# Performance work log

Measured on AMD Instinct MI355X. Metric: run time of the kernel, lower is better.

Reference implementation:

```python
import jax, jax.numpy as jnp
import numpy as np

WS = 7      # window size
NH = 8      # num heads

def setup_inputs() -> dict:
    key = jax.random.key(0)
    k1, k2, k3 = jax.random.split(key, 3)
    B, H, W, C = 32, 56, 56, 256
    x = jax.random.normal(k1, (B, H, W, C), dtype=jnp.float32)
    w_qkv = jax.random.normal(k2, (3 * C, C), dtype=jnp.float32) * 0.02
    w_proj = jax.random.normal(k3, (C, C), dtype=jnp.float32) * 0.02
    b_proj = jnp.zeros((C,), dtype=jnp.float32)
    return {"x": x, "w_qkv": w_qkv, "w_proj": w_proj, "b_proj": b_proj}

def reference(x, w_qkv, w_proj, b_proj):
    B, H, W, C = x.shape
    hd = C // NH
    scale = hd ** -0.5
    # window partition: (B,H,W,C) -> (nW, ws^2, C)
    xw = x.reshape(B, H // WS, WS, W // WS, WS, C)
    xw = xw.transpose(0, 1, 3, 2, 4, 5).reshape(-1, WS * WS, C)
    # fused qkv projection (no bias)
    qkv = (xw @ w_qkv.T).reshape(-1, WS * WS, 3, NH, hd)
    q, k, v = qkv[:, :, 0], qkv[:, :, 1], qkv[:, :, 2]  # (nW, ws^2, nh, hd)
    # NOTE: faithful to source quirk — contraction over head_dim per token,
    # producing an (nh x nh) head-mixing attention matrix per token.
    attn = jnp.einsum('nshd,nsed->nshe', q, k) * scale   # (nW, ws^2, nh, nh)
    attn = jax.nn.softmax(attn, axis=-1)
    out = jnp.einsum('nshe,nsed->nshd', attn, v)         # (nW, ws^2, nh, hd)
    # source does transpose(1,2).reshape(-1, ws^2, C) — replicate exactly
    out = out.swapaxes(1, 2).reshape(-1, WS * WS, C)
    out = out @ w_proj.T + b_proj
    # window un-partition
    out = out.reshape(B, H // WS, W // WS, WS, WS, C)
    out = out.transpose(0, 1, 3, 2, 4, 5).reshape(B, H, W, C)
    return out
```

## Files before the change

### kernel.cpp

```cpp
#include <hip/hip_runtime.h>
#include <hip/hip_bf16.h>

typedef __bf16 bf16_t;
typedef bf16_t bf16x8 __attribute__((ext_vector_type(8)));
typedef float floatx4 __attribute__((ext_vector_type(4)));

#define MFMA16(a, b, c) __builtin_amdgcn_mfma_f32_16x16x32_bf16((a), (b), (c), 0, 0, 0)

__global__ __launch_bounds__(256) void wconv_kernel(
    const float* __restrict__ w_qkv, const float* __restrict__ w_proj,
    bf16_t* __restrict__ wb)
{
  int i = blockIdx.x * 256 + threadIdx.x;
  const float* src;
  bf16_t* dst;
  if (i < 24576) {
    int chunk = i >> 6, l = i & 63;
    int p = chunk >> 5, rem = chunk & 31, k = rem >> 2, j = rem & 3;
    int col = p * 64 + j * 16 + (l & 15);
    int kk = k * 32 + (l >> 4) * 8;
    src = w_qkv + col * 256 + kk;
    dst = wb + (i << 3);
  } else {
    int ip = i - 24576;
    int chunk = ip >> 6, l = ip & 63;
    int p = chunk >> 4, rem = chunk & 15, k = rem >> 1, j = rem & 1;
    int col = p * 32 + j * 16 + (l & 15);
    int kk = k * 32 + (l >> 4) * 8;
    src = w_proj + col * 256 + kk;
    dst = wb + 196608 + (ip << 3);
  }
  float4 f0 = ((const float4*)src)[0];
  float4 f1 = ((const float4*)src)[1];
  bf16_t t8[8] = {(bf16_t)f0.x, (bf16_t)f0.y, (bf16_t)f0.z, (bf16_t)f0.w,
                  (bf16_t)f1.x, (bf16_t)f1.y, (bf16_t)f1.z, (bf16_t)f1.w};
  *(uint4*)dst = *(const uint4*)t8;
}

__device__ __forceinline__ void cvt8_store(bf16_t* dst, float4 f0, float4 f1) {
  bf16_t t8[8] = {(bf16_t)f0.x, (bf16_t)f0.y, (bf16_t)f0.z, (bf16_t)f0.w,
                  (bf16_t)f1.x, (bf16_t)f1.y, (bf16_t)f1.z, (bf16_t)f1.w};
  *(uint4*)dst = *(const uint4*)t8;
}

#define XS_S 272
#define QK_S 520

__global__ __launch_bounds__(512, 4) void attn_kernel(
    const float* __restrict__ x,
    const bf16_t* __restrict__ wb,
    float* __restrict__ outf,
    bf16_t* __restrict__ preb)
{
  __shared__ __align__(16) bf16_t Xs[32][XS_S];
  __shared__ __align__(16) bf16_t QK[32][QK_S];

  const int tid = threadIdx.x;
  const int wave = tid >> 6, lane = tid & 63, quad = lane >> 4, l16 = lane & 15;
  const long base = (long)blockIdx.x * 32;
  const float scale = 0.17677669529663687f;

  auto loadB = [&](bf16x8* dst, int pan, int k) {
    const bf16_t* c = wb + ((long)(pan * 32 + k * 4) << 9) + lane * 8;
#pragma unroll
    for (int j = 0; j < 4; ++j) dst[j] = *(const bf16x8*)(c + (j << 9));
  };

  const float* xb = x + base * 256;
#pragma unroll
  for (int it = 0; it < 2; ++it) {
    int idx = tid + it * 512;
    int s = idx >> 5, g = (idx & 31) * 8;
    const float* p = xb + s * 256 + g;
    float4 f0 = ((const float4*)p)[0];
    float4 f1 = ((const float4*)p)[1];
    cvt8_store(&Xs[s][g], f0, f1);
  }
  __syncthreads();

  {
    floatx4 acc[2][4] = {};
    bf16x8 Ba[4], Bb[4];
    loadB(Ba, wave, 0);
#pragma unroll
    for (int k = 0; k < 8; ++k) {
      const bf16x8* cur = (k & 1) ? Bb : Ba;
      if (k < 7) loadB((k & 1) ? Ba : Bb, wave, k + 1);
      bf16x8 A0 = *(const bf16x8*)(&Xs[l16][k * 32 + quad * 8]);
      bf16x8 A1 = *(const bf16x8*)(&Xs[16 + l16][k * 32 + quad * 8]);
#pragma unroll
      for (int j = 0; j < 4; ++j) {
        acc[0][j] = MFMA16(A0, cur[j], acc[0][j]);
        acc[1][j] = MFMA16(A1, cur[j], acc[1][j]);
      }
    }
#pragma unroll
    for (int i = 0; i < 2; ++i)
#pragma unroll
      for (int j = 0; j < 4; ++j)
#pragma unroll
        for (int r = 0; r < 4; ++r)
          QK[i * 16 + quad * 4 + r][wave * 64 + j * 16 + l16] = (bf16_t)acc[i][j][r];
  }
  __syncthreads();

  float p_[8];
  floatx4 vacc[2][4];
  if (wave < 4) {
    const int t = tid >> 3, h = tid & 7;
    bf16x8 qv[4];
#pragma unroll
    for (int u = 0; u < 4; ++u) qv[u] = *(const bf16x8*)(&QK[t][h * 32 + u * 8]);
    float qf[32];
#pragma unroll
    for (int u = 0; u < 4; ++u)
#pragma unroll
      for (int d = 0; d < 8; ++d) qf[u * 8 + d] = (float)qv[u][d];
    float sc[8];
#pragma unroll
    for (int eh = 0; eh < 2; ++eh) {
      bf16x8 kv[4][4];
#pragma unroll
      for (int e2 = 0; e2 < 4; ++e2)
#pragma unroll
        for (int u = 0; u < 4; ++u)
          kv[e2][u] = *(const bf16x8*)(&QK[t][256 + (eh * 4 + e2) * 32 + u * 8]);
#pragma unroll
      for (int e2 = 0; e2 < 4; ++e2) {
        float a = 0.f;
#pragma unroll
        for (int u = 0; u < 4; ++u)
#pragma unroll
          for (int d = 0; d < 8; ++d) a += qf[u * 8 + d] * (float)kv[e2][u][d];
        sc[eh * 4 + e2] = a;
      }
    }
    float mx = -INFINITY;
#pragma unroll
    for (int e = 0; e < 8; ++e) { sc[e] *= scale; mx = fmaxf(mx, sc[e]); }
    float sum = 0.f;
#pragma unroll
    for (int e = 0; e < 8; ++e) { p_[e] = __expf(sc[e] - mx); sum += p_[e]; }
    float rs = 1.0f / sum;
#pragma unroll
    for (int e = 0; e < 8; ++e) p_[e] *= rs;
  } else {
    const int pan = 8 + (wave - 4);
#pragma unroll
    for (int i = 0; i < 2; ++i)
#pragma unroll
      for (int j = 0; j < 4; ++j) vacc[i][j] = (floatx4){0.f, 0.f, 0.f, 0.f};
    bf16x8 Ba[4], Bb[4];
    loadB(Ba, pan, 0);
#pragma unroll
    for (int k = 0; k < 8; ++k) {
      const bf16x8* cur = (k & 1) ? Bb : Ba;
      if (k < 7) loadB((k & 1) ? Ba : Bb, pan, k + 1);
      bf16x8 A0 = *(const bf16x8*)(&Xs[l16][k * 32 + quad * 8]);
      bf16x8 A1 = *(const bf16x8*)(&Xs[16 + l16][k * 32 + quad * 8]);
#pragma unroll
      for (int j = 0; j < 4; ++j) {
        vacc[0][j] = MFMA16(A0, cur[j], vacc[0][j]);
        vacc[1][j] = MFMA16(A1, cur[j], vacc[1][j]);
      }
    }
  }
  __syncthreads();

  if (wave >= 4) {
    const int u = wave - 4;
#pragma unroll
    for (int i = 0; i < 2; ++i)
#pragma unroll
      for (int j = 0; j < 4; ++j)
#pragma unroll
        for (int r = 0; r < 4; ++r)
          QK[i * 16 + quad * 4 + r][u * 64 + j * 16 + l16] = (bf16_t)vacc[i][j][r];
  }
  __syncthreads();

  if (wave < 4) {
    const int t = tid >> 3, h = tid & 7;
    float pre[32];
#pragma unroll
    for (int i = 0; i < 32; ++i) pre[i] = 0.f;
#pragma unroll
    for (int eh = 0; eh < 2; ++eh) {
      bf16x8 vv[4][4];
#pragma unroll
      for (int e2 = 0; e2 < 4; ++e2)
#pragma unroll
        for (int u = 0; u < 4; ++u)
          vv[e2][u] = *(const bf16x8*)(&QK[t][(eh * 4 + e2) * 32 + u * 8]);
#pragma unroll
      for (int e2 = 0; e2 < 4; ++e2) {
        float pe = p_[eh * 4 + e2];
#pragma unroll
        for (int u = 0; u < 4; ++u)
#pragma unroll
          for (int d = 0; d < 8; ++d) pre[u * 8 + d] += pe * (float)vv[e2][u][d];
      }
    }
    if (preb) {
      bf16_t* op = preb + (base + t) * 256 + h * 32;
#pragma unroll
      for (int u = 0; u < 4; ++u) {
        bf16_t t8[8];
#pragma unroll
        for (int d = 0; d < 8; ++d) t8[d] = (bf16_t)pre[u * 8 + d];
        *(uint4*)(op + u * 8) = *(const uint4*)t8;
      }
    } else {
      float* op = outf + (base + t) * 256 + h * 32;
#pragma unroll
      for (int u = 0; u < 8; ++u) {
        float4 f = {pre[u * 4], pre[u * 4 + 1], pre[u * 4 + 2], pre[u * 4 + 3]};
        ((float4*)op)[u] = f;
      }
    }
  }
}

#define SC_S 264

__global__ __launch_bounds__(512, 4) void proj_kernel(
    const bf16_t* __restrict__ wb,
    const float* __restrict__ b_proj,
    float* out,
    const bf16_t* __restrict__ preb)
{
  __shared__ __align__(16) bf16_t Sc[49][SC_S];
  __shared__ int trow[49];

  const int n = blockIdx.x;
  const int b = n >> 6, wh = (n >> 3) & 7, ww = n & 7;
  const int tid = threadIdx.x;
  const int wave = tid >> 6, lane = tid & 63, quad = lane >> 4, l16 = lane & 15;

  auto loadB2 = [&](bf16x8 (*dst)[2], int k0) {
#pragma unroll
    for (int kk = 0; kk < 4; ++kk)
#pragma unroll
      for (int j = 0; j < 2; ++j)
        dst[kk][j] = *(const bf16x8*)(wb + 196608 +
            ((long)(wave * 16 + (k0 + kk) * 2 + j) << 9) + lane * 8);
  };
  bf16x8 Bh0[4][2];
  loadB2(Bh0, 0);
  float bv[2];
#pragma unroll
  for (int j = 0; j < 2; ++j) bv[j] = b_proj[wave * 32 + j * 16 + l16];

  if (tid < 49) {
    int i = tid / 7, j = tid % 7;
    trow[tid] = b * 3136 + (wh * 7 + i) * 56 + ww * 7 + j;
  }
  __syncthreads();

  if (preb) {
    for (int idx = tid; idx < 49 * 32; idx += 512) {
      int s = idx >> 5, g8 = idx & 31;
      bf16x8 v = *(const bf16x8*)(preb + (long)trow[s] * 256 + g8 * 8);
      int flat = (g8 >> 2) * 1568 + s * 32 + (g8 & 3) * 8;
      *(bf16x8*)(&Sc[flat >> 8][flat & 255]) = v;
    }
  } else {
    for (int idx = tid; idx < 49 * 32; idx += 512) {
      int s = idx >> 5, g8 = idx & 31;
      const float* p = out + (long)trow[s] * 256 + g8 * 8;
      float4 f0 = ((const float4*)p)[0];
      float4 f1 = ((const float4*)p)[1];
      int flat = (g8 >> 2) * 1568 + s * 32 + (g8 & 3) * 8;
      cvt8_store(&Sc[flat >> 8][flat & 255], f0, f1);
    }
  }
  bf16x8 Bh1[4][2];
  loadB2(Bh1, 4);
  __syncthreads();

  {
    floatx4 acc[4][2] = {};
    bf16x8 Aa[4], Ab[4];
    auto loadA = [&](bf16x8* dst, int k) {
#pragma unroll
      for (int i = 0; i < 4; ++i) {
        int mr = i * 16 + l16; if (mr > 48) mr = 48;
        dst[i] = *(const bf16x8*)(&Sc[mr][k * 32 + quad * 8]);
      }
    };
    loadA(Aa, 0);
#pragma unroll
    for (int k = 0; k < 8; ++k) {
      const bf16x8* curA = (k & 1) ? Ab : Aa;
      if (k < 7) loadA((k & 1) ? Aa : Ab, k + 1);
#pragma unroll
      for (int i = 0; i < 4; ++i)
#pragma unroll
        for (int j = 0; j < 2; ++j)
          acc[i][j] = MFMA16(curA[i], (k < 4) ? Bh0[k][j] : Bh1[k - 4][j], acc[i][j]);
    }
#pragma unroll
    for (int j = 0; j < 2; ++j) {
      int col = wave * 32 + j * 16 + l16;
#pragma unroll
      for (int i = 0; i < 4; ++i)
#pragma unroll
        for (int r = 0; r < 4; ++r) {
          int m = i * 16 + quad * 4 + r;
          if (m < 49) out[(long)trow[m] * 256 + col] = acc[i][j][r] + bv[j];
        }
    }
  }
}

extern "C" void kernel_launch(void* const* d_in, const int* in_sizes, int n_in,
                              void* d_out, int out_size, void* d_ws, size_t ws_size,
                              hipStream_t stream) {
  (void)in_sizes; (void)n_in; (void)out_size;
  const float* x      = (const float*)d_in[0];
  const float* w_qkv  = (const float*)d_in[1];
  const float* w_proj = (const float*)d_in[2];
  const float* b_proj = (const float*)d_in[3];
  float* out = (float*)d_out;
  bf16_t* wb = (bf16_t*)d_ws;

  bf16_t* preb = nullptr;
  if (ws_size >= (size_t)524288 + 51380224) preb = wb + 262144;

  wconv_kernel<<<dim3(128), 256, 0, stream>>>(w_qkv, w_proj, wb);
  attn_kernel<<<dim3(3136), 512, 0, stream>>>(x, wb, out, preb);
  proj_kernel<<<dim3(2048), 512, 0, stream>>>(wb, b_proj, out, preb);
}
```

Measured before the change: 279.9 us.

## Compute QKV in one MFMA pass, split head-mix across lanes, gather proj A directly

The attention kernel now has all 8 waves compute 96 of the 768 QKV columns each in a single GEMM pass, with V written into the reused Xs buffer. This replaces the earlier split where half the waves idled during the V GEMM. The head-mixing softmax is split across two lanes per (token, head) using a shuffle reduction, and the probabilities are stored in shared memory as fp16. The P·V step is spread across all 512 threads instead of only 256. The projection kernel drops the shared-memory staging and gathers its A operands straight from the bf16 intermediate with the transposed indexing, at the cost of scattered global loads and per-element division arithmetic.

```diff
diff --git a/kernel.cpp b/kernel.cpp
--- a/kernel.cpp
+++ b/kernel.cpp
@@ -16,8 +16,8 @@
   bf16_t* dst;
   if (i < 24576) {
     int chunk = i >> 6, l = i & 63;
-    int p = chunk >> 5, rem = chunk & 31, k = rem >> 2, j = rem & 3;
-    int col = p * 64 + j * 16 + (l & 15);
+    int c = chunk >> 3, k = chunk & 7;
+    int col = c * 16 + (l & 15);
     int kk = k * 32 + (l >> 4) * 8;
     src = w_qkv + col * 256 + kk;
     dst = wb + (i << 3);
@@ -43,7 +43,7 @@
   *(uint4*)dst = *(const uint4*)t8;
 }
 
-#define XS_S 272
+#define XS_S 264
 #define QK_S 520
 
 __global__ __launch_bounds__(512, 4) void attn_kernel(
@@ -54,17 +54,12 @@
 {
   __shared__ __align__(16) bf16_t Xs[32][XS_S];
   __shared__ __align__(16) bf16_t QK[32][QK_S];
+  __shared__ __align__(16) _Float16 Pl[32][8][8];
 
   const int tid = threadIdx.x;
   const int wave = tid >> 6, lane = tid & 63, quad = lane >> 4, l16 = lane & 15;
   const long base = (long)blockIdx.x * 32;
   const float scale = 0.17677669529663687f;
-
-  auto loadB = [&](bf16x8* dst, int pan, int k) {
-    const bf16_t* c = wb + ((long)(pan * 32 + k * 4) << 9) + lane * 8;
-#pragma unroll
-    for (int j = 0; j < 4; ++j) dst[j] = *(const bf16x8*)(c + (j << 9));
-  };
 
   const float* xb = x + base * 256;
 #pragma unroll
@@ -78,239 +73,274 @@
   }
   __syncthreads();
 
+  floatx4 acc[2][6];
+#pragma unroll
+  for (int i = 0; i < 2; ++i)
+#pragma unroll
+    for (int j = 0; j < 6; ++j) acc[i][j] = (floatx4){0.f, 0.f, 0.f, 0.f};
   {
-    floatx4 acc[2][4] = {};
-    bf16x8 Ba[4], Bb[4];
-    loadB(Ba, wave, 0);
+    auto loadB6 = [&](bf16x8 (&dst)[6], int k) {
+      const bf16_t* cb = wb + ((long)(wave * 48 + k) << 9) + lane * 8;
+#pragma unroll
+      for (int j = 0; j < 6; ++j) dst[j] = *(const bf16x8*)(cb + (j << 12));
+    };
+    bf16x8 Ba[6], Bb[6];
+    loadB6(Ba, 0);
 #pragma unroll
     for (int k = 0; k < 8; ++k) {
       const bf16x8* cur = (k & 1) ? Bb : Ba;
-      if (k < 7) loadB((k & 1) ? Ba : Bb, wave, k + 1);
+      if (k < 7) loadB6((k & 1) ? Ba : Bb, k + 1);
       bf16x8 A0 = *(const bf16x8*)(&Xs[l16][k * 32 + quad * 8]);
       bf16x8 A1 = *(const bf16x8*)(&Xs[16 + l16][k * 32 + quad * 8]);
 #pragma unroll
-      for (int j = 0; j < 4; ++j) {
+      for (int j = 0; j < 6; ++j) {
         acc[0][j] = MFMA16(A0, cur[j], acc[0][j]);
         acc[1][j] = MFMA16(A1, cur[j], acc[1][j]);
       }
     }
+  }
+  __syncthreads();
+
+#pragma unroll
+  for (int j = 0; j < 6; ++j) {
+    int g = wave * 96 + j * 16 + l16;
 #pragma unroll
     for (int i = 0; i < 2; ++i)
 #pragma unroll
-      for (int j = 0; j < 4; ++j)
-#pragma unroll
-        for (int r = 0; r < 4; ++r)
-          QK[i * 16 + quad * 4 + r][wave * 64 + j * 16 + l16] = (bf16_t)acc[i][j][r];
-  }
-  __syncthreads();
-
-  float p_[8];
-  floatx4 vacc[2][4];
-  if (wave < 4) {
-    const int t = tid >> 3, h = tid & 7;
-    bf16x8 qv[4];
-#pragma unroll
-    for (int u = 0; u < 4; ++u) qv[u] = *(const bf16x8*)(&QK[t][h * 32 + u * 8]);
-    float qf[32];
-#pragma unroll
-    for (int u = 0; u < 4; ++u)
-#pragma unroll
-      for (int d = 0; d < 8; ++d) qf[u * 8 + d] = (float)qv[u][d];
+      for (int r = 0; r < 4; ++r) {
+        int row = i * 16 + quad * 4 + r;
+        if (g < 512) QK[row][g] = (bf16_t)acc[i][j][r];
+        else         Xs[row][g - 512] = (bf16_t)acc[i][j][r];
+      }
+  }
+  __syncthreads();
+
+  {
+    const int t = tid >> 4, h = (tid >> 1) & 7, sg = tid & 1;
+    const bf16_t* qrow = &QK[t][h * 32 + sg * 16];
+    float qf[16];
+    {
+      bf16x8 q0 = *(const bf16x8*)(qrow);
+      bf16x8 q1 = *(const bf16x8*)(qrow + 8);
+#pragma unroll
+      for (int d = 0; d < 8; ++d) { qf[d] = (float)q0[d]; qf[8 + d] = (float)q1[d]; }
+    }
     float sc[8];
 #pragma unroll
-    for (int eh = 0; eh < 2; ++eh) {
-      bf16x8 kv[4][4];
-#pragma unroll
-      for (int e2 = 0; e2 < 4; ++e2)
-#pragma unroll
-        for (int u = 0; u < 4; ++u)
-          kv[e2][u] = *(const bf16x8*)(&QK[t][256 + (eh * 4 + e2) * 32 + u * 8]);
-#pragma unroll
-      for (int e2 = 0; e2 < 4; ++e2) {
-        float a = 0.f;
-#pragma unroll
-        for (int u = 0; u < 4; ++u)
-#pragma unroll
-          for (int d = 0; d < 8; ++d) a += qf[u * 8 + d] * (float)kv[e2][u][d];
-        sc[eh * 4 + e2] = a;
-      }
-    }
+    for (int e = 0; e < 8; ++e) {
+      const bf16_t* krow = &QK[t][256 + e * 32 + sg * 16];
+      bf16x8 k0 = *(const bf16x8*)(krow);
+      bf16x8 k1 = *(const bf16x8*)(krow + 8);
+      float a = 0.f;
+#pragma unroll
+      for (int d = 0; d < 8; ++d) a += qf[d] * (float)k0[d] + qf[8 + d] * (float)k1[d];
+      sc[e] = a;
+    }
+#pragma unroll
+    for (int e = 0; e < 8; ++e) sc[e] += __shfl_xor(sc[e], 1);
     float mx = -INFINITY;
 #pragma unroll
     for (int e = 0; e < 8; ++e) { sc[e] *= scale; mx = fmaxf(mx, sc[e]); }
-    float sum = 0.f;
-#pragma unroll
-    for (int e = 0; e < 8; ++e) { p_[e] = __expf(sc[e] - mx); sum += p_[e]; }
+    float sum = 0.f, pv[8];
+#pragma unroll
+    for (int e = 0; e < 8; ++e) { pv[e] = __expf(sc[e] - mx); sum += pv[e]; }
     float rs = 1.0f / sum;
-#pragma unroll
-    for (int e = 0; e < 8; ++e) p_[e] *= rs;
-  } else {
-    const int pan = 8 + (wave - 4);
-#pragma unroll
-    for (int i = 0; i < 2; ++i)
-#pragma unroll
-      for (int j = 0; j < 4; ++j) vacc[i][j] = (floatx4){0.f, 0.f, 0.f, 0.f};
-    bf16x8 Ba[4], Bb[4];
-    loadB(Ba, pan, 0);
-#pragma unroll
-    for (int k = 0; k < 8; ++k) {
-      const bf16x8* cur = (k & 1) ? Bb : Ba;
-      if (k < 7) loadB((k & 1) ? Ba : Bb, pan, k + 1);
-      bf16x8 A0 = *(const bf16x8*)(&Xs[l16][k * 32 + quad * 8]);
-      bf16x8 A1 = *(const bf16x8*)(&Xs[16 + l16][k * 32 + quad * 8]);
-#pragma unroll
-      for (int j = 0; j < 4; ++j) {
-        vacc[0][j] = MFMA16(A0, cur[j], vacc[0][j]);
-        vacc[1][j] = MFMA16(A1, cur[j], vacc[1][j]);
-      }
-    }
-  }
-  __syncthreads();
-
-  if (wave >= 4) {
-    const int u = wave - 4;
-#pragma unroll
-    for (int i = 0; i < 2; ++i)
-#pragma unroll
-      for (int j = 0; j < 4; ++j)
-#pragma unroll
-        for (int r = 0; r < 4; ++r)
-          QK[i * 16 + quad * 4 + r][u * 64 + j * 16 + l16] = (bf16_t)vacc[i][j][r];
-  }
-  __syncthreads();
-
-  if (wave < 4) {
-    const int t = tid >> 3, h = tid & 7;
-    float pre[32];
-#pragma unroll
-    for (int i = 0; i < 32; ++i) pre[i] = 0.f;
-#pragma unroll
-    for (int eh = 0; eh < 2; ++eh) {
-      bf16x8 vv[4][4];
-#pragma unroll
-      for (int e2 = 0; e2 < 4; ++e2)
-#pragma unroll
-        for (int u = 0; u < 4; ++u)
-          vv[e2][u] = *(const bf16x8*)(&QK[t][(eh * 4 + e2) * 32 + u * 8]);
-#pragma unroll
-      for (int e2 = 0; e2 < 4; ++e2) {
-        float pe = p_[eh * 4 + e2];
-#pragma unroll
-        for (int u = 0; u < 4; ++u)
-#pragma unroll
-          for (int d = 0; d < 8; ++d) pre[u * 8 + d] += pe * (float)vv[e2][u][d];
+    if (sg == 0) {
+      _Float16 ph[8];
+#pragma unroll
+      for (int e = 0; e < 8; ++e) ph[e] = (_Float16)(pv[e] * rs);
+      *(uint4*)(&Pl[t][h][0]) = *(const uint4*)ph;
+    }
+  }
+  __syncthreads();
+
+  {
+    const int t = tid >> 4, j = tid & 15, j8 = j & 7, h0 = j >> 3;
+    float pf[4][8];
+#pragma unroll
+    for (int m = 0; m < 4; ++m) {
+      _Float16 ph[8];
+      *(uint4*)ph = *(const uint4*)(&Pl[t][h0 + 2 * m][0]);
+#pragma unroll
+      for (int e = 0; e < 8; ++e) pf[m][e] = (float)ph[e];
+    }
+    float pr[4][4];
+#pragma unroll
+    for (int m = 0; m < 4; ++m)
+#pragma unroll
+      for (int d = 0; d < 4; ++d) pr[m][d] = 0.f;
+#pragma unroll
+    for (int e = 0; e < 8; ++e) {
+      bf16_t v4[4];
+      *(uint2*)v4 = *(const uint2*)(&Xs[t][e * 32 + j8 * 4]);
+      float vf[4];
+#pragma unroll
+      for (int d = 0; d < 4; ++d) vf[d] = (float)v4[d];
+#pragma unroll
+      for (int m = 0; m < 4; ++m) {
+        float pe = pf[m][e];
+#pragma unroll
+        for (int d = 0; d < 4; ++d) pr[m][d] += pe * vf[d];
       }
     }
     if (preb) {
-      bf16_t* op = preb + (base + t) * 256 + h * 32;
-#pragma unroll
-      for (int u = 0; u < 4; ++u) {
-        bf16_t t8[8];
-#pragma unroll
-        for (int d = 0; d < 8; ++d) t8[d] = (bf16_t)pre[u * 8 + d];
-        *(uint4*)(op + u * 8) = *(const uint4*)t8;
+      bf16_t* op = preb + (base + t) * 256 + j * 4;
+#pragma unroll
+      for (int m = 0; m < 4; ++m) {
+        bf16_t o4[4] = {(bf16_t)pr[m][0], (bf16_t)pr[m][1],
+                        (bf16_t)pr[m][2], (bf16_t)pr[m][3]};
+        *(uint2*)(op + m * 64) = *(const uint2*)o4;
       }
     } else {
-      float* op = outf + (base + t) * 256 + h * 32;
-#pragma unroll
-      for (int u = 0; u < 8; ++u) {
-        float4 f = {pre[u * 4], pre[u * 4 + 1], pre[u * 4 + 2], pre[u * 4 + 3]};
-        ((float4*)op)[u] = f;
-      }
-    }
-  }
-}
-
-#define SC_S 264
+      float* op = outf + (base + t) * 256 + j * 4;
+#pragma unroll
+      for (int m = 0; m < 4; ++m) {
+        float4 f = {pr[m][0], pr[m][1], pr[m][2], pr[m][3]};
+        *(float4*)(op + m * 64) = f;
+      }
+    }
+  }
+}
 
 __global__ __launch_bounds__(512, 4) void proj_kernel(
     const bf16_t* __restrict__ wb,
     const float* __restrict__ b_proj,
-    float* out,
+    float* __restrict__ out,
     const bf16_t* __restrict__ preb)
+{
+  const int n = blockIdx.x;
+  const int b = n >> 6, wh = (n >> 3) & 7, ww = n & 7;
+  const int rowbase = b * 3136 + wh * 392 + ww * 7;
+  const int tid = threadIdx.x;
+  const int wave = tid >> 6, lane = tid & 63, quad = lane >> 4, l16 = lane & 15;
+
+  auto loadBp = [&](bf16x8 (&dst)[2], int k) {
+#pragma unroll
+    for (int j = 0; j < 2; ++j)
+      dst[j] = *(const bf16x8*)(wb + 196608 +
+          ((long)(wave * 16 + k * 2 + j) << 9) + lane * 8);
+  };
+  auto loadA = [&](bf16x8 (&dst)[4], int k) {
+#pragma unroll
+    for (int i = 0; i < 4; ++i) {
+      int mr = i * 16 + l16; if (mr > 48) mr = 48;
+      int q5 = mr * 8 + k;
+      int h = q5 / 49;
+      int s = q5 - h * 49;
+      int srow = (s / 7) * 56 + (s - (s / 7) * 7);
+      dst[i] = *(const bf16x8*)(preb + (long)(rowbase + srow) * 256 +
+                                h * 32 + quad * 8);
+    }
+  };
+
+  const float bv0 = b_proj[wave * 32 + l16];
+  const float bv1 = b_proj[wave * 32 + 16 + l16];
+
+  floatx4 acc[4][2];
+#pragma unroll
+  for (int i = 0; i < 4; ++i)
+#pragma unroll
+    for (int j = 0; j < 2; ++j) acc[i][j] = (floatx4){0.f, 0.f, 0.f, 0.f};
+
+  bf16x8 Aa[4], Ab[4], Ba[2], Bb[2];
+  loadA(Aa, 0); loadBp(Ba, 0);
+#pragma unroll
+  for (int k = 0; k < 8; ++k) {
+    const bf16x8* cA = (k & 1) ? Ab : Aa;
+    const bf16x8* cB = (k & 1) ? Bb : Ba;
+    if (k < 7) { loadA((k & 1) ? Aa : Ab, k + 1); loadBp((k & 1) ? Ba : Bb, k + 1); }
+#pragma unroll
+    for (int i = 0; i < 4; ++i) {
+      acc[i][0] = MFMA16(cA[i], cB[0], acc[i][0]);
+      acc[i][1] = MFMA16(cA[i], cB[1], acc[i][1]);
+    }
+  }
+#pragma unroll
+  for (int i = 0; i < 4; ++i)
+#pragma unroll
+    for (int r = 0; r < 4; ++r) {
+      int m = i * 16 + quad * 4 + r;
+      if (m < 49) {
+        int srow = (m / 7) * 56 + (m - (m / 7) * 7);
+        float* orow = out + (long)(rowbase + srow) * 256 + wave * 32 + l16;
+        orow[0]  = acc[i][0][r] + bv0;
+        orow[16] = acc[i][1][r] + bv1;
+      }
+    }
+}
+
+#define SC_S 264
+__global__ __launch_bounds__(512, 4) void proj_fallback(
+    const bf16_t* __restrict__ wb,
+    const float* __restrict__ b_proj,
+    float* out)
 {
   __shared__ __align__(16) bf16_t Sc[49][SC_S];
   __shared__ int trow[49];
-
   const int n = blockIdx.x;
   const int b = n >> 6, wh = (n >> 3) & 7, ww = n & 7;
   const int tid = threadIdx.x;
   const int wave = tid >> 6, lane = tid & 63, quad = lane >> 4, l16 = lane & 15;
 
-  auto loadB2 = [&](bf16x8 (*dst)[2], int k0) {
-#pragma unroll
-    for (int kk = 0; kk < 4; ++kk)
-#pragma unroll
-      for (int j = 0; j < 2; ++j)
-        dst[kk][j] = *(const bf16x8*)(wb + 196608 +
-            ((long)(wave * 16 + (k0 + kk) * 2 + j) << 9) + lane * 8);
+  auto loadBp = [&](bf16x8 (&dst)[2], int k) {
+#pragma unroll
+    for (int j = 0; j < 2; ++j)
+      dst[j] = *(const bf16x8*)(wb + 196608 +
+          ((long)(wave * 16 + k * 2 + j) << 9) + lane * 8);
   };
-  bf16x8 Bh0[4][2];
-  loadB2(Bh0, 0);
-  float bv[2];
-#pragma unroll
-  for (int j = 0; j < 2; ++j) bv[j] = b_proj[wave * 32 + j * 16 + l16];
+  const float bv0 = b_proj[wave * 32 + l16];
+  const float bv1 = b_proj[wave * 32 + 16 + l16];
 
   if (tid < 49) {
     int i = tid / 7, j = tid % 7;
     trow[tid] = b * 3136 + (wh * 7 + i) * 56 + ww * 7 + j;
   }
   __syncthreads();
-
-  if (preb) {
-    for (int idx = tid; idx < 49 * 32; idx += 512) {
-      int s = idx >> 5, g8 = idx & 31;
-      bf16x8 v = *(const bf16x8*)(preb + (long)trow[s] * 256 + g8 * 8);
-      int flat = (g8 >> 2) * 1568 + s * 32 + (g8 & 3) * 8;
-      *(bf16x8*)(&Sc[flat >> 8][flat & 255]) = v;
-    }
-  } else {
-    for (int idx = tid; idx < 49 * 32; idx += 512) {
-      int s = idx >> 5, g8 = idx & 31;
-      const float* p = out + (long)trow[s] * 256 + g8 * 8;
-      float4 f0 = ((const float4*)p)[0];
-      float4 f1 = ((const float4*)p)[1];
-      int flat = (g8 >> 2) * 1568 + s * 32 + (g8 & 3) * 8;
-      cvt8_store(&Sc[flat >> 8][flat & 255], f0, f1);
-    }
-  }
-  bf16x8 Bh1[4][2];
-  loadB2(Bh1, 4);
-  __syncthreads();
-
-  {
-    floatx4 acc[4][2] = {};
-    bf16x8 Aa[4], Ab[4];
-    auto loadA = [&](bf16x8* dst, int k) {
-#pragma unroll
-      for (int i = 0; i < 4; ++i) {
-        int mr = i * 16 + l16; if (mr > 48) mr = 48;
-        dst[i] = *(const bf16x8*)(&Sc[mr][k * 32 + quad * 8]);
-      }
-    };
-    loadA(Aa, 0);
-#pragma unroll
-    for (int k = 0; k < 8; ++k) {
-      const bf16x8* curA = (k & 1) ? Ab : Aa;
-      if (k < 7) loadA((k & 1) ? Aa : Ab, k + 1);
-#pragma unroll
-      for (int i = 0; i < 4; ++i)
-#pragma unroll
-        for (int j = 0; j < 2; ++j)
-          acc[i][j] = MFMA16(curA[i], (k < 4) ? Bh0[k][j] : Bh1[k - 4][j], acc[i][j]);
-    }
-#pragma unroll
-    for (int j = 0; j < 2; ++j) {
-      int col = wave * 32 + j * 16 + l16;
-#pragma unroll
-      for (int i = 0; i < 4; ++i)
-#pragma unroll
-        for (int r = 0; r < 4; ++r) {
-          int m = i * 16 + quad * 4 + r;
-          if (m < 49) out[(long)trow[m] * 256 + col] = acc[i][j][r] + bv[j];
-        }
-    }
-  }
+  for (int idx = tid; idx < 49 * 32; idx += 512) {
+    int s = idx >> 5, c8 = idx & 31;
+    const float* p = out + (long)trow[s] * 256 + c8 * 8;
+    float4 f0 = ((const float4*)p)[0];
+    float4 f1 = ((const float4*)p)[1];
+    int flat = (c8 >> 2) * 1568 + s * 32 + (c8 & 3) * 8;
+    cvt8_store(&Sc[flat >> 8][flat & 255], f0, f1);
+  }
+  __syncthreads();
+  floatx4 acc[4][2];
+#pragma unroll
+  for (int i = 0; i < 4; ++i)
+#pragma unroll
+    for (int j = 0; j < 2; ++j) acc[i][j] = (floatx4){0.f, 0.f, 0.f, 0.f};
+  bf16x8 Aa[4], Ab[4], Ba[2], Bb[2];
+  auto loadA = [&](bf16x8* dst, int k) {
+#pragma unroll
+    for (int i = 0; i < 4; ++i) {
+      int mr = i * 16 + l16; if (mr > 48) mr = 48;
+      dst[i] = *(const bf16x8*)(&Sc[mr][k * 32 + quad * 8]);
+    }
+  };
+  loadA(Aa, 0); loadBp(Ba, 0);
+#pragma unroll
+  for (int k = 0; k < 8; ++k) {
+    const bf16x8* cA = (k & 1) ? Ab : Aa;
+    const bf16x8* cB = (k & 1) ? Bb : Ba;
+    if (k < 7) { loadA((k & 1) ? Aa : Ab, k + 1); loadBp((k & 1) ? Ba : Bb, k + 1); }
+#pragma unroll
+    for (int i = 0; i < 4; ++i) {
+      acc[i][0] = MFMA16(cA[i], cB[0], acc[i][0]);
+      acc[i][1] = MFMA16(cA[i], cB[1], acc[i][1]);
+    }
+  }
+#pragma unroll
+  for (int i = 0; i < 4; ++i)
+#pragma unroll
+    for (int r = 0; r < 4; ++r) {
+      int m = i * 16 + quad * 4 + r;
+      if (m < 49) {
+        float* orow = out + (long)trow[m] * 256 + wave * 32 + l16;
+        orow[0]  = acc[i][0][r] + bv0;
+        orow[16] = acc[i][1][r] + bv1;
+      }
+    }
 }
 
 extern "C" void kernel_launch(void* const* d_in, const int* in_sizes, int n_in,
@@ -329,5 +359,8 @@
 
   wconv_kernel<<<dim3(128), 256, 0, stream>>>(w_qkv, w_proj, wb);
   attn_kernel<<<dim3(3136), 512, 0, stream>>>(x, wb, out, preb);
-  proj_kernel<<<dim3(2048), 512, 0, stream>>>(wb, b_proj, out, preb);
-}
+  if (preb)
+    proj_kernel<<<dim3(2048), 512, 0, stream>>>(wb, b_proj, out, preb);
+  else
+    proj_fallback<<<dim3(2048), 512, 0, stream>>>(wb, b_proj, out);
+}
```

After: 293.7 us. 1.05x slower.
